# Kernel tuning notes

Hardware: AMD Instinct MI355X
Metric: run time of the kernel (lower is better)

The kernel has to match this reference:

```python
import jax, jax.numpy as jnp
import numpy as np

NUM_LAYERS = 3
CHANNELS = 8
IN_CHANNELS = 8
MASK_OUT_STRIDE = 4
WEIGHT_NUMS = [(IN_CHANNELS + 2) * CHANNELS, CHANNELS * CHANNELS, CHANNELS]
BIAS_NUMS = [CHANNELS, CHANNELS, 1]
NUM_GEN_PARAMS = sum(WEIGHT_NUMS) + sum(BIAS_NUMS)  # 169
SOI = np.array([64.0, 128.0, 256.0, 512.0, 1024.0], dtype=np.float32)


def compute_locations(h, w, stride):
    # FCOS grid point centers, (H*W, 2) in (x, y) order
    shifts_x = jnp.arange(w, dtype=jnp.float32) * stride + stride // 2
    shifts_y = jnp.arange(h, dtype=jnp.float32) * stride + stride // 2
    ys, xs = jnp.meshgrid(shifts_y, shifts_x, indexing='ij')
    return jnp.stack([xs.reshape(-1), ys.reshape(-1)], axis=1)


def parse_dynamic_params(params):
    # params: (n_inst, 169) -> per-layer weights (n, cout, cin) and biases (n, cout)
    n = params.shape[0]
    split_pts = np.cumsum(WEIGHT_NUMS + BIAS_NUMS)[:-1].tolist()
    splits = jnp.split(params, split_pts, axis=1)
    ws, bs = [], []
    for l in range(NUM_LAYERS):
        cout = CHANNELS if l < NUM_LAYERS - 1 else 1
        ws.append(splits[l].reshape(n, cout, -1))
        bs.append(splits[NUM_LAYERS + l].reshape(n, cout))
    return ws, bs


def aligned_bilinear(x, factor):
    # Faithful port of AdelaiDet aligned_bilinear (replicate pad + align_corners=True bilinear).
    if factor == 1:
        return x
    n, c, h, w = x.shape
    xp = jnp.pad(x, ((0, 0), (0, 0), (0, 1), (0, 1)), mode='edge')  # (n,c,h+1,w+1)
    oh, ow = factor * h + 1, factor * w + 1
    # align_corners=True with oh = factor*h+1 over h+1 samples -> exact coords i/factor
    ys = jnp.arange(oh, dtype=x.dtype) / factor
    xs = jnp.arange(ow, dtype=x.dtype) / factor
    y0 = jnp.floor(ys).astype(jnp.int32)
    y1 = jnp.minimum(y0 + 1, h)
    x0 = jnp.floor(xs).astype(jnp.int32)
    x1 = jnp.minimum(x0 + 1, w)
    wy = (ys - y0.astype(x.dtype))[None, None, :, None]
    wx = (xs - x0.astype(x.dtype))[None, None, None, :]
    rows = xp[:, :, y0, :] * (1 - wy) + xp[:, :, y1, :] * wy
    out = rows[:, :, :, x0] * (1 - wx) + rows[:, :, :, x1] * wx
    pad = factor // 2
    out = jnp.pad(out, ((0, 0), (0, 0), (pad, 0), (pad, 0)), mode='edge')
    return out[:, :, :oh - 1, :ow - 1]  # (n, c, factor*h, factor*w)


def dynamic_head(x, params):
    # x: (n_inst, cin, HW); per-instance 1x1 convs == batched tiny GEMMs
    ws, bs = parse_dynamic_params(params)
    h = x
    for i, (w, b) in enumerate(zip(ws, bs)):
        h = jnp.einsum('noi,nip->nop', w, h) + b[:, :, None]
        if i < NUM_LAYERS - 1:
            h = jax.nn.relu(h)
    return h  # (n_inst, 1, HW)


def setup_inputs() -> dict:
    key = jax.random.key(0)
    k = jax.random.split(key, 6)
    N, H, W, n_inst = 2, 200, 200, 128
    return {
        'mask_feats': jax.random.normal(k[0], (N, IN_CHANNELS, H, W), jnp.float32),
        'mask_head_params': jax.random.normal(k[1], (n_inst, NUM_GEN_PARAMS), jnp.float32) * 0.1,
        'boundary_head_params': jax.random.normal(k[2], (n_inst, NUM_GEN_PARAMS), jnp.float32) * 0.1,
        'instance_locations': jax.random.uniform(k[3], (n_inst, 2), jnp.float32) * 1600.0,
        'im_inds': jax.random.randint(k[4], (n_inst,), 0, N),
        'fpn_levels': jax.random.randint(k[5], (n_inst,), 0, 5),
        'mask_feat_stride': 8,
    }


def reference(mask_feats, mask_head_params, boundary_head_params, instance_locations, im_inds, fpn_levels, mask_feat_stride):
    N, C, H, W = mask_feats.shape
    n_inst = mask_head_params.shape[0]
    locs = compute_locations(H, W, mask_feat_stride)                 # (HW, 2)
    rel = instance_locations[:, None, :] - locs[None, :, :]          # (n, HW, 2)
    rel = jnp.transpose(rel, (0, 2, 1))                              # (n, 2, HW)
    soi = jnp.asarray(SOI)[fpn_levels]                               # (n,)
    rel = (rel / soi[:, None, None]).astype(mask_feats.dtype)
    feats = mask_feats[im_inds].reshape(n_inst, C, H * W)            # per-instance gather
    x = jnp.concatenate([rel, feats], axis=1)                        # (n, C+2, HW)
    factor = mask_feat_stride // MASK_OUT_STRIDE
    m = aligned_bilinear(dynamic_head(x, mask_head_params).reshape(n_inst, 1, H, W), factor)
    bd = aligned_bilinear(dynamic_head(x, boundary_head_params).reshape(n_inst, 1, H, W), factor)
    return jax.nn.sigmoid(m), jax.nn.sigmoid(bd)
```

## Files before the change

### kernel.cpp

```cpp
#include <hip/hip_runtime.h>


#define BLOCK 256
#define Hh 200
#define Ww 200
#define NP 169
#define TH 25
#define MAXR 14
#define OW 400
#define OH 400

typedef float f32x4 __attribute__((ext_vector_type(4)));
typedef float f32x2 __attribute__((ext_vector_type(2)));
typedef _Float16 f16x4 __attribute__((ext_vector_type(4)));

__device__ __forceinline__ f32x2 splat2(float v) { f32x2 r; r.x = v; r.y = v; return r; }
__device__ __forceinline__ f32x2 pkfma(f32x2 a, f32x2 b, f32x2 c) {
    return __builtin_elementwise_fma(a, b, c);
}

__global__ __launch_bounds__(BLOCK, 4) void dmh_fused(
    const float* __restrict__ mask_feats,
    const float* __restrict__ mparams,
    const float* __restrict__ bparams,
    const float* __restrict__ ilocs,
    const int*   __restrict__ im_inds,
    const int*   __restrict__ fpn_levels,
    const int*   __restrict__ stride_p,
    float* __restrict__ out,
    int n_inst)
{
    __shared__ __align__(16) float s_par[2 * 192];
    __shared__ __align__(16) _Float16 s_m[2][MAXR][Ww];

    const int tid  = threadIdx.x;
    const int tile = blockIdx.x;
    const int inst = blockIdx.y;

    for (int j = tid; j < 2 * NP; j += BLOCK) {
        const int head = (j < NP) ? 0 : 1;
        const int k = j - head * NP;
        const float v = head ? bparams[inst * NP + k] : mparams[inst * NP + k];
        int dst;
        if      (k < 80)  dst = (k / 10) * 12 + (k % 10);
        else if (k < 144) dst = 96 + (k - 80);
        else if (k < 152) dst = 160 + (k - 144);
        else if (k < 160) dst = 168 + (k - 152);
        else if (k < 168) dst = 176 + (k - 160);
        else              dst = 184;
        s_par[head * 192 + dst] = v;
    }

    const int   s    = stride_p[0];
    const int   half = s >> 1;
    const int   im   = im_inds[inst];
    const int   lvl  = fpn_levels[inst];
    const float inv_soi = 1.0f / (float)(64 << lvl);
    const float ixl = ilocs[inst * 2 + 0];
    const float iyl = ilocs[inst * 2 + 1];

    const int i0 = tile * TH;
    const int r_begin = ((i0 > 0) ? (i0 - 1) : 0) >> 1;
    int r_end = ((i0 + TH - 2) >> 1) + 1;
    if (r_end > Hh - 1) r_end = Hh - 1;
    const int nrows = r_end - r_begin + 1;

    __syncthreads();

    const int npx = nrows * Ww;
    const float* fbase = mask_feats + (size_t)im * 8 * Hh * Ww;

    for (int g = tid * 4; g < npx; g += BLOCK * 4) {
        asm volatile("" ::: "memory");

        const int lr = g / Ww;
        const int c  = g - lr * Ww;
        const int r  = r_begin + lr;

        f32x2 xa[10], xb[10];
        {
            const float ry   = (iyl - (float)(r * s + half)) * inv_soi;
            const float step = -(float)s * inv_soi;
            const float cx0  = (ixl - (float)(c * s + half)) * inv_soi;
            xa[0].x = cx0;            xa[0].y = cx0 + step;
            xb[0].x = cx0 + 2*step;   xb[0].y = cx0 + 3*step;
            xa[1] = splat2(ry);       xb[1] = xa[1];
            const float* fp = fbase + r * Ww + c;
            #pragma unroll
            for (int ch = 0; ch < 8; ch++) {
                const f32x4 f = *(const f32x4*)(fp + ch * (Hh * Ww));
                xa[2 + ch].x = f.x; xa[2 + ch].y = f.y;
                xb[2 + ch].x = f.z; xb[2 + ch].y = f.w;
            }
        }

        #pragma unroll 1
        for (int head = 0; head < 2; head++) {
            const float* P = s_par + head * 192;
            const f32x2 zero = splat2(0.0f);

            f32x2 h1a[8], h1b[8];
            #pragma unroll
            for (int o = 0; o < 8; o++) {
                const f32x4 wa = *(const f32x4*)(P + o * 12);
                const f32x4 wb = *(const f32x4*)(P + o * 12 + 4);
                const float w8 = P[o * 12 + 8];
                const float w9 = P[o * 12 + 9];
                f32x2 aa = splat2(P[168 + o]);
                f32x2 ab = aa;
                aa = pkfma(splat2(wa.x), xa[0], aa); ab = pkfma(splat2(wa.x), xb[0], ab);
                aa = pkfma(splat2(wa.y), xa[1], aa); ab = pkfma(splat2(wa.y), xb[1], ab);
                aa = pkfma(splat2(wa.z), xa[2], aa); ab = pkfma(splat2(wa.z), xb[2], ab);
                aa = pkfma(splat2(wa.w), xa[3], aa); ab = pkfma(splat2(wa.w), xb[3], ab);
                aa = pkfma(splat2(wb.x), xa[4], aa); ab = pkfma(splat2(wb.x), xb[4], ab);
                aa = pkfma(splat2(wb.y), xa[5], aa); ab = pkfma(splat2(wb.y), xb[5], ab);
                aa = pkfma(splat2(wb.z), xa[6], aa); ab = pkfma(splat2(wb.z), xb[6], ab);
                aa = pkfma(splat2(wb.w), xa[7], aa); ab = pkfma(splat2(wb.w), xb[7], ab);
                aa = pkfma(splat2(w8),   xa[8], aa); ab = pkfma(splat2(w8),   xb[8], ab);
                aa = pkfma(splat2(w9),   xa[9], aa); ab = pkfma(splat2(w9),   xb[9], ab);
                h1a[o] = __builtin_elementwise_max(aa, zero);
                h1b[o] = __builtin_elementwise_max(ab, zero);
            }

            f32x2 h2a[8], h2b[8];
            #pragma unroll
            for (int o = 0; o < 8; o++) {
                const f32x4 wa = *(const f32x4*)(P + 96 + o * 8);
                const f32x4 wb = *(const f32x4*)(P + 96 + o * 8 + 4);
                f32x2 aa = splat2(P[176 + o]);
                f32x2 ab = aa;
                aa = pkfma(splat2(wa.x), h1a[0], aa); ab = pkfma(splat2(wa.x), h1b[0], ab);
                aa = pkfma(splat2(wa.y), h1a[1], aa); ab = pkfma(splat2(wa.y), h1b[1], ab);
                aa = pkfma(splat2(wa.z), h1a[2], aa); ab = pkfma(splat2(wa.z), h1b[2], ab);
                aa = pkfma(splat2(wa.w), h1a[3], aa); ab = pkfma(splat2(wa.w), h1b[3], ab);
                aa = pkfma(splat2(wb.x), h1a[4], aa); ab = pkfma(splat2(wb.x), h1b[4], ab);
                aa = pkfma(splat2(wb.y), h1a[5], aa); ab = pkfma(splat2(wb.y), h1b[5], ab);
                aa = pkfma(splat2(wb.z), h1a[6], aa); ab = pkfma(splat2(wb.z), h1b[6], ab);
                aa = pkfma(splat2(wb.w), h1a[7], aa); ab = pkfma(splat2(wb.w), h1b[7], ab);
                h2a[o] = __builtin_elementwise_max(aa, zero);
                h2b[o] = __builtin_elementwise_max(ab, zero);
            }

            const f32x4 wa = *(const f32x4*)(P + 160);
            const f32x4 wb = *(const f32x4*)(P + 164);
            f32x2 aa = splat2(P[184]);
            f32x2 ab = aa;
            aa = pkfma(splat2(wa.x), h2a[0], aa); ab = pkfma(splat2(wa.x), h2b[0], ab);
            aa = pkfma(splat2(wa.y), h2a[1], aa); ab = pkfma(splat2(wa.y), h2b[1], ab);
            aa = pkfma(splat2(wa.z), h2a[2], aa); ab = pkfma(splat2(wa.z), h2b[2], ab);
            aa = pkfma(splat2(wa.w), h2a[3], aa); ab = pkfma(splat2(wa.w), h2b[3], ab);
            aa = pkfma(splat2(wb.x), h2a[4], aa); ab = pkfma(splat2(wb.x), h2b[4], ab);
            aa = pkfma(splat2(wb.y), h2a[5], aa); ab = pkfma(splat2(wb.y), h2b[5], ab);
            aa = pkfma(splat2(wb.z), h2a[6], aa); ab = pkfma(splat2(wb.z), h2b[6], ab);
            aa = pkfma(splat2(wb.w), h2a[7], aa); ab = pkfma(splat2(wb.w), h2b[7], ab);

            f16x4 res;
            res.x = (_Float16)aa.x; res.y = (_Float16)aa.y;
            res.z = (_Float16)ab.x; res.w = (_Float16)ab.y;
            *(f16x4*)(&s_m[head][lr][c]) = res;
        }
    }

    __syncthreads();

    float* out0 = out + (size_t)inst * (OH * OW) + (size_t)i0 * OW;
    float* out1 = out0 + (size_t)n_inst * (OH * OW);

    const float C = -1.44269504f;
    const int NU = OW / 8;
    const int ntaskb = TH * NU;
    for (int t = tid; t < ntaskb; t += BLOCK) {
        const int row = t / NU;
        const int u   = t - row * NU;
        const int i   = i0 + row;
        const int ip  = (i > 0) ? (i - 1) : 0;
        const int y0  = ip >> 1;
        const float wy = (ip & 1) ? 0.5f : 0.0f;
        const int lr0 = y0 - r_begin;
        const int r1c = (y0 + 1 <= Hh - 1) ? (y0 + 1) : (Hh - 1);
        const int lr1 = r1c - r_begin;

        #pragma unroll
        for (int head = 0; head < 2; head++) {
            const f16x4 A0h = *(const f16x4*)(&s_m[head][lr0][4 * u]);
            const f16x4 A1h = *(const f16x4*)(&s_m[head][lr1][4 * u]);
            float p0 = 0.0f, p1 = 0.0f;
            if (u > 0) {
                p0 = (float)s_m[head][lr0][4 * u - 1];
                p1 = (float)s_m[head][lr1][4 * u - 1];
            }
            float Bv[4];
            #pragma unroll
            for (int m = 0; m < 4; m++) {
                const float a0 = (float)A0h[m], a1 = (float)A1h[m];
                Bv[m] = (a0 + (a1 - a0) * wy) * C;
            }
            const float PB = (p0 + (p1 - p0) * wy) * C;

            float e[8];
            e[0] = (u > 0) ? 0.5f * (PB + Bv[0]) : Bv[0];
            e[1] = Bv[0];
            e[2] = 0.5f * (Bv[0] + Bv[1]);
            e[3] = Bv[1];
            e[4] = 0.5f * (Bv[1] + Bv[2]);
            e[5] = Bv[2];
            e[6] = 0.5f * (Bv[2] + Bv[3]);
            e[7] = Bv[3];

            f32x4 lo, hi;
            #pragma unroll
            for (int k = 0; k < 4; k++) {
                lo[k] = __builtin_amdgcn_rcpf(1.0f + __builtin_amdgcn_exp2f(e[k]));
                hi[k] = __builtin_amdgcn_rcpf(1.0f + __builtin_amdgcn_exp2f(e[4 + k]));
            }

            float* dst = (head ? out1 : out0) + row * OW + 8 * u;
            __builtin_nontemporal_store(lo, (f32x4*)dst);
            __builtin_nontemporal_store(hi, (f32x4*)(dst + 4));
        }
    }
}

extern "C" void kernel_launch(void* const* d_in, const int* in_sizes, int n_in,
                              void* d_out, int out_size, void* d_ws, size_t ws_size,
                              hipStream_t stream) {
    const float* mask_feats = (const float*)d_in[0];
    const float* mparams    = (const float*)d_in[1];
    const float* bparams    = (const float*)d_in[2];
    const float* ilocs      = (const float*)d_in[3];
    const int*   im_inds    = (const int*)d_in[4];
    const int*   fpn_levels = (const int*)d_in[5];
    const int*   stride_p   = (const int*)d_in[6];
    float* out = (float*)d_out;

    const int n_inst = in_sizes[1] / NP;
    dim3 grid(OH / TH, n_inst);
    dim3 block(BLOCK);
    hipLaunchKernelGGL(dmh_fused, grid, block, 0, stream,
                       mask_feats, mparams, bparams, ilocs,
                       im_inds, fpn_levels, stride_p, out, n_inst);
}
```

Before: 65.28 us.

## Split fused kernel into MLP pass and upsample pass via fp16 workspace

Replaces the single fused kernel, which recomputed halo rows of the low-res MLP output per tile, with two kernels. The first evaluates both dynamic-head MLPs once per low-res pixel and writes fp16 results to the workspace. The second performs the bilinear upsample and sigmoid from that buffer. This removes the redundant halo MLP work and the block-level barriers, at the cost of an extra launch and a global round-trip of the intermediate. The fused kernel remains as a fallback when the workspace is too small.

```diff
diff --git a/kernel.cpp b/kernel.cpp
--- a/kernel.cpp
+++ b/kernel.cpp
@@ -17,6 +17,202 @@
 __device__ __forceinline__ f32x2 splat2(float v) { f32x2 r; r.x = v; r.y = v; return r; }
 __device__ __forceinline__ f32x2 pkfma(f32x2 a, f32x2 b, f32x2 c) {
     return __builtin_elementwise_fma(a, b, c);
+}
+
+__device__ __forceinline__ int park_dst(int k) {
+    if (k < 80)  return (k / 10) * 12 + (k % 10);
+    if (k < 144) return 96 + (k - 80);
+    if (k < 152) return 160 + (k - 144);
+    if (k < 160) return 168 + (k - 152);
+    if (k < 168) return 176 + (k - 160);
+    return 184;
+}
+
+__device__ __forceinline__ void mlp4(const float* __restrict__ P,
+    const f32x2 (&xa)[10], const f32x2 (&xb)[10], f32x2& oa_, f32x2& ob_)
+{
+    const f32x2 zero = splat2(0.0f);
+
+    f32x2 h1a[8], h1b[8];
+    #pragma unroll
+    for (int o = 0; o < 8; o++) {
+        const f32x4 wa = *(const f32x4*)(P + o * 12);
+        const f32x4 wb = *(const f32x4*)(P + o * 12 + 4);
+        const float w8 = P[o * 12 + 8];
+        const float w9 = P[o * 12 + 9];
+        f32x2 aa = splat2(P[168 + o]);
+        f32x2 ab = aa;
+        aa = pkfma(splat2(wa.x), xa[0], aa); ab = pkfma(splat2(wa.x), xb[0], ab);
+        aa = pkfma(splat2(wa.y), xa[1], aa); ab = pkfma(splat2(wa.y), xb[1], ab);
+        aa = pkfma(splat2(wa.z), xa[2], aa); ab = pkfma(splat2(wa.z), xb[2], ab);
+        aa = pkfma(splat2(wa.w), xa[3], aa); ab = pkfma(splat2(wa.w), xb[3], ab);
+        aa = pkfma(splat2(wb.x), xa[4], aa); ab = pkfma(splat2(wb.x), xb[4], ab);
+        aa = pkfma(splat2(wb.y), xa[5], aa); ab = pkfma(splat2(wb.y), xb[5], ab);
+        aa = pkfma(splat2(wb.z), xa[6], aa); ab = pkfma(splat2(wb.z), xb[6], ab);
+        aa = pkfma(splat2(wb.w), xa[7], aa); ab = pkfma(splat2(wb.w), xb[7], ab);
+        aa = pkfma(splat2(w8),   xa[8], aa); ab = pkfma(splat2(w8),   xb[8], ab);
+        aa = pkfma(splat2(w9),   xa[9], aa); ab = pkfma(splat2(w9),   xb[9], ab);
+        h1a[o] = __builtin_elementwise_max(aa, zero);
+        h1b[o] = __builtin_elementwise_max(ab, zero);
+    }
+
+    f32x2 h2a[8], h2b[8];
+    #pragma unroll
+    for (int o = 0; o < 8; o++) {
+        const f32x4 wa = *(const f32x4*)(P + 96 + o * 8);
+        const f32x4 wb = *(const f32x4*)(P + 96 + o * 8 + 4);
+        f32x2 aa = splat2(P[176 + o]);
+        f32x2 ab = aa;
+        aa = pkfma(splat2(wa.x), h1a[0], aa); ab = pkfma(splat2(wa.x), h1b[0], ab);
+        aa = pkfma(splat2(wa.y), h1a[1], aa); ab = pkfma(splat2(wa.y), h1b[1], ab);
+        aa = pkfma(splat2(wa.z), h1a[2], aa); ab = pkfma(splat2(wa.z), h1b[2], ab);
+        aa = pkfma(splat2(wa.w), h1a[3], aa); ab = pkfma(splat2(wa.w), h1b[3], ab);
+        aa = pkfma(splat2(wb.x), h1a[4], aa); ab = pkfma(splat2(wb.x), h1b[4], ab);
+        aa = pkfma(splat2(wb.y), h1a[5], aa); ab = pkfma(splat2(wb.y), h1b[5], ab);
+        aa = pkfma(splat2(wb.z), h1a[6], aa); ab = pkfma(splat2(wb.z), h1b[6], ab);
+        aa = pkfma(splat2(wb.w), h1a[7], aa); ab = pkfma(splat2(wb.w), h1b[7], ab);
+        h2a[o] = __builtin_elementwise_max(aa, zero);
+        h2b[o] = __builtin_elementwise_max(ab, zero);
+    }
+
+    const f32x4 wa = *(const f32x4*)(P + 160);
+    const f32x4 wb = *(const f32x4*)(P + 164);
+    f32x2 aa = splat2(P[184]);
+    f32x2 ab = aa;
+    aa = pkfma(splat2(wa.x), h2a[0], aa); ab = pkfma(splat2(wa.x), h2b[0], ab);
+    aa = pkfma(splat2(wa.y), h2a[1], aa); ab = pkfma(splat2(wa.y), h2b[1], ab);
+    aa = pkfma(splat2(wa.z), h2a[2], aa); ab = pkfma(splat2(wa.z), h2b[2], ab);
+    aa = pkfma(splat2(wa.w), h2a[3], aa); ab = pkfma(splat2(wa.w), h2b[3], ab);
+    aa = pkfma(splat2(wb.x), h2a[4], aa); ab = pkfma(splat2(wb.x), h2b[4], ab);
+    aa = pkfma(splat2(wb.y), h2a[5], aa); ab = pkfma(splat2(wb.y), h2b[5], ab);
+    aa = pkfma(splat2(wb.z), h2a[6], aa); ab = pkfma(splat2(wb.z), h2b[6], ab);
+    aa = pkfma(splat2(wb.w), h2a[7], aa); ab = pkfma(splat2(wb.w), h2b[7], ab);
+    oa_ = aa; ob_ = ab;
+}
+
+__global__ __launch_bounds__(BLOCK, 4) void dmh_mlp(
+    const float* __restrict__ mask_feats,
+    const float* __restrict__ mparams,
+    const float* __restrict__ bparams,
+    const float* __restrict__ ilocs,
+    const int*   __restrict__ im_inds,
+    const int*   __restrict__ fpn_levels,
+    const int*   __restrict__ stride_p,
+    _Float16* __restrict__ mbuf)
+{
+    __shared__ __align__(16) float s_par[2 * 192];
+    const int tid   = threadIdx.x;
+    const int strip = blockIdx.x;
+    const int inst  = blockIdx.y;
+
+    for (int j = tid; j < 2 * NP; j += BLOCK) {
+        const int head = (j < NP) ? 0 : 1;
+        const int k = j - head * NP;
+        const float v = head ? bparams[inst * NP + k] : mparams[inst * NP + k];
+        s_par[head * 192 + park_dst(k)] = v;
+    }
+
+    const int   s    = stride_p[0];
+    const int   half = s >> 1;
+    const int   im   = im_inds[inst];
+    const int   lvl  = fpn_levels[inst];
+    const float inv_soi = 1.0f / (float)(64 << lvl);
+    const float ixl = ilocs[inst * 2 + 0];
+    const float iyl = ilocs[inst * 2 + 1];
+
+    __syncthreads();
+    if (tid >= 250) return;
+
+    const int px = strip * 1000 + tid * 4;
+    const int r  = px / 200;
+    const int c  = px - r * 200;
+    const float* fbase = mask_feats + (size_t)im * 8 * Hh * Ww;
+
+    f32x2 xa[10], xb[10];
+    {
+        const float ry   = (iyl - (float)(r * s + half)) * inv_soi;
+        const float step = -(float)s * inv_soi;
+        const float cx0  = (ixl - (float)(c * s + half)) * inv_soi;
+        xa[0].x = cx0;            xa[0].y = cx0 + step;
+        xb[0].x = cx0 + 2*step;   xb[0].y = cx0 + 3*step;
+        xa[1] = splat2(ry);       xb[1] = xa[1];
+        const float* fp = fbase + r * Ww + c;
+        #pragma unroll
+        for (int ch = 0; ch < 8; ch++) {
+            const f32x4 f = *(const f32x4*)(fp + ch * (Hh * Ww));
+            xa[2 + ch].x = f.x; xa[2 + ch].y = f.y;
+            xb[2 + ch].x = f.z; xb[2 + ch].y = f.w;
+        }
+    }
+
+    #pragma unroll 1
+    for (int head = 0; head < 2; head++) {
+        f32x2 oa, ob;
+        mlp4(s_par + head * 192, xa, xb, oa, ob);
+        f16x4 res;
+        res.x = (_Float16)oa.x; res.y = (_Float16)oa.y;
+        res.z = (_Float16)ob.x; res.w = (_Float16)ob.y;
+        *(f16x4*)(mbuf + ((size_t)(inst * 2 + head) * 40000 + r * 200 + c)) = res;
+    }
+}
+
+__global__ __launch_bounds__(BLOCK, 4) void dmh_upsample(
+    const _Float16* __restrict__ mbuf,
+    float* __restrict__ out, int n_inst)
+{
+    const int t = blockIdx.x * BLOCK + threadIdx.x;
+    if (t >= n_inst * 20000) return;
+    const int inst = t / 20000;
+    const int rem  = t - inst * 20000;
+    const int row  = rem / 50;
+    const int u    = rem - row * 50;
+
+    const int ip = (row > 0) ? (row - 1) : 0;
+    const int y0 = ip >> 1;
+    const int y1 = (y0 + 1 <= Hh - 1) ? (y0 + 1) : (Hh - 1);
+    const float wy = (ip & 1) ? 0.5f : 0.0f;
+    const float C = -1.44269504f;
+
+    float* out0 = out + (size_t)inst * (OH * OW) + row * OW + 8 * u;
+    float* out1 = out0 + (size_t)n_inst * (OH * OW);
+
+    #pragma unroll
+    for (int head = 0; head < 2; head++) {
+        const _Float16* m0 = mbuf + ((size_t)(inst * 2 + head) * 40000 + y0 * 200);
+        const _Float16* m1 = mbuf + ((size_t)(inst * 2 + head) * 40000 + y1 * 200);
+        const f16x4 A0 = *(const f16x4*)(m0 + 4 * u);
+        const f16x4 A1 = *(const f16x4*)(m1 + 4 * u);
+        float p0 = 0.0f, p1 = 0.0f;
+        if (u > 0) { p0 = (float)m0[4 * u - 1]; p1 = (float)m1[4 * u - 1]; }
+
+        float Bv[4];
+        #pragma unroll
+        for (int m = 0; m < 4; m++) {
+            const float a0 = (float)A0[m], a1 = (float)A1[m];
+            Bv[m] = (a0 + (a1 - a0) * wy) * C;
+        }
+        const float PB = (p0 + (p1 - p0) * wy) * C;
+
+        float e[8];
+        e[0] = (u > 0) ? 0.5f * (PB + Bv[0]) : Bv[0];
+        e[1] = Bv[0];
+        e[2] = 0.5f * (Bv[0] + Bv[1]);
+        e[3] = Bv[1];
+        e[4] = 0.5f * (Bv[1] + Bv[2]);
+        e[5] = Bv[2];
+        e[6] = 0.5f * (Bv[2] + Bv[3]);
+        e[7] = Bv[3];
+
+        f32x4 lo, hi;
+        #pragma unroll
+        for (int k = 0; k < 4; k++) {
+            lo[k] = __builtin_amdgcn_rcpf(1.0f + __builtin_amdgcn_exp2f(e[k]));
+            hi[k] = __builtin_amdgcn_rcpf(1.0f + __builtin_amdgcn_exp2f(e[4 + k]));
+        }
+        float* dst = head ? out1 : out0;
+        __builtin_nontemporal_store(lo, (f32x4*)dst);
+        __builtin_nontemporal_store(hi, (f32x4*)(dst + 4));
+    }
 }
 
 __global__ __launch_bounds__(BLOCK, 4) void dmh_fused(
@@ -41,14 +237,7 @@
         const int head = (j < NP) ? 0 : 1;
         const int k = j - head * NP;
         const float v = head ? bparams[inst * NP + k] : mparams[inst * NP + k];
-        int dst;
-        if      (k < 80)  dst = (k / 10) * 12 + (k % 10);
-        else if (k < 144) dst = 96 + (k - 80);
-        else if (k < 152) dst = 160 + (k - 144);
-        else if (k < 160) dst = 168 + (k - 152);
-        else if (k < 168) dst = 176 + (k - 160);
-        else              dst = 184;
-        s_par[head * 192 + dst] = v;
+        s_par[head * 192 + park_dst(k)] = v;
     }
 
     const int   s    = stride_p[0];
@@ -72,7 +261,6 @@
 
     for (int g = tid * 4; g < npx; g += BLOCK * 4) {
         asm volatile("" ::: "memory");
-
         const int lr = g / Ww;
         const int c  = g - lr * Ww;
         const int r  = r_begin + lr;
@@ -96,67 +284,11 @@
 
         #pragma unroll 1
         for (int head = 0; head < 2; head++) {
-            const float* P = s_par + head * 192;
-            const f32x2 zero = splat2(0.0f);
-
-            f32x2 h1a[8], h1b[8];
-            #pragma unroll
-            for (int o = 0; o < 8; o++) {
-                const f32x4 wa = *(const f32x4*)(P + o * 12);
-                const f32x4 wb = *(const f32x4*)(P + o * 12 + 4);
-                const float w8 = P[o * 12 + 8];
-                const float w9 = P[o * 12 + 9];
-                f32x2 aa = splat2(P[168 + o]);
-                f32x2 ab = aa;
-                aa = pkfma(splat2(wa.x), xa[0], aa); ab = pkfma(splat2(wa.x), xb[0], ab);
-                aa = pkfma(splat2(wa.y), xa[1], aa); ab = pkfma(splat2(wa.y), xb[1], ab);
-                aa = pkfma(splat2(wa.z), xa[2], aa); ab = pkfma(splat2(wa.z), xb[2], ab);
-                aa = pkfma(splat2(wa.w), xa[3], aa); ab = pkfma(splat2(wa.w), xb[3], ab);
-                aa = pkfma(splat2(wb.x), xa[4], aa); ab = pkfma(splat2(wb.x), xb[4], ab);
-                aa = pkfma(splat2(wb.y), xa[5], aa); ab = pkfma(splat2(wb.y), xb[5], ab);
-                aa = pkfma(splat2(wb.z), xa[6], aa); ab = pkfma(splat2(wb.z), xb[6], ab);
-                aa = pkfma(splat2(wb.w), xa[7], aa); ab = pkfma(splat2(wb.w), xb[7], ab);
-                aa = pkfma(splat2(w8),   xa[8], aa); ab = pkfma(splat2(w8),   xb[8], ab);
-                aa = pkfma(splat2(w9),   xa[9], aa); ab = pkfma(splat2(w9),   xb[9], ab);
-                h1a[o] = __builtin_elementwise_max(aa, zero);
-                h1b[o] = __builtin_elementwise_max(ab, zero);
-            }
-
-            f32x2 h2a[8], h2b[8];
-            #pragma unroll
-            for (int o = 0; o < 8; o++) {
-                const f32x4 wa = *(const f32x4*)(P + 96 + o * 8);
-                const f32x4 wb = *(const f32x4*)(P + 96 + o * 8 + 4);
-                f32x2 aa = splat2(P[176 + o]);
-                f32x2 ab = aa;
-                aa = pkfma(splat2(wa.x), h1a[0], aa); ab = pkfma(splat2(wa.x), h1b[0], ab);
-                aa = pkfma(splat2(wa.y), h1a[1], aa); ab = pkfma(splat2(wa.y), h1b[1], ab);
-                aa = pkfma(splat2(wa.z), h1a[2], aa); ab = pkfma(splat2(wa.z), h1b[2], ab);
-                aa = pkfma(splat2(wa.w), h1a[3], aa); ab = pkfma(splat2(wa.w), h1b[3], ab);
-                aa = pkfma(splat2(wb.x), h1a[4], aa); ab = pkfma(splat2(wb.x), h1b[4], ab);
-                aa = pkfma(splat2(wb.y), h1a[5], aa); ab = pkfma(splat2(wb.y), h1b[5], ab);
-                aa = pkfma(splat2(wb.z), h1a[6], aa); ab = pkfma(splat2(wb.z), h1b[6], ab);
-                aa = pkfma(splat2(wb.w), h1a[7], aa); ab = pkfma(splat2(wb.w), h1b[7], ab);
-                h2a[o] = __builtin_elementwise_max(aa, zero);
-                h2b[o] = __builtin_elementwise_max(ab, zero);
-            }
-
-            const f32x4 wa = *(const f32x4*)(P + 160);
-            const f32x4 wb = *(const f32x4*)(P + 164);
-            f32x2 aa = splat2(P[184]);
-            f32x2 ab = aa;
-            aa = pkfma(splat2(wa.x), h2a[0], aa); ab = pkfma(splat2(wa.x), h2b[0], ab);
-            aa = pkfma(splat2(wa.y), h2a[1], aa); ab = pkfma(splat2(wa.y), h2b[1], ab);
-            aa = pkfma(splat2(wa.z), h2a[2], aa); ab = pkfma(splat2(wa.z), h2b[2], ab);
-            aa = pkfma(splat2(wa.w), h2a[3], aa); ab = pkfma(splat2(wa.w), h2b[3], ab);
-            aa = pkfma(splat2(wb.x), h2a[4], aa); ab = pkfma(splat2(wb.x), h2b[4], ab);
-            aa = pkfma(splat2(wb.y), h2a[5], aa); ab = pkfma(splat2(wb.y), h2b[5], ab);
-            aa = pkfma(splat2(wb.z), h2a[6], aa); ab = pkfma(splat2(wb.z), h2b[6], ab);
-            aa = pkfma(splat2(wb.w), h2a[7], aa); ab = pkfma(splat2(wb.w), h2b[7], ab);
-
+            f32x2 oa, ob;
+            mlp4(s_par + head * 192, xa, xb, oa, ob);
             f16x4 res;
-            res.x = (_Float16)aa.x; res.y = (_Float16)aa.y;
-            res.z = (_Float16)ab.x; res.w = (_Float16)ab.y;
+            res.x = (_Float16)oa.x; res.y = (_Float16)oa.y;
+            res.z = (_Float16)ob.x; res.w = (_Float16)ob.y;
             *(f16x4*)(&s_m[head][lr][c]) = res;
         }
     }
@@ -234,9 +366,20 @@
     float* out = (float*)d_out;
 
     const int n_inst = in_sizes[1] / NP;
-    dim3 grid(OH / TH, n_inst);
-    dim3 block(BLOCK);
-    hipLaunchKernelGGL(dmh_fused, grid, block, 0, stream,
-                       mask_feats, mparams, bparams, ilocs,
-                       im_inds, fpn_levels, stride_p, out, n_inst);
-}
+    const size_t need = (size_t)n_inst * 2 * 40000 * sizeof(_Float16);
+
+    if (ws_size >= need) {
+        _Float16* mbuf = (_Float16*)d_ws;
+        hipLaunchKernelGGL(dmh_mlp, dim3(40, n_inst), dim3(BLOCK), 0, stream,
+                           mask_feats, mparams, bparams, ilocs,
+                           im_inds, fpn_levels, stride_p, mbuf);
+        const int ntask = n_inst * 20000;
+        hipLaunchKernelGGL(dmh_upsample, dim3((ntask + BLOCK - 1) / BLOCK),
+                           dim3(BLOCK), 0, stream, mbuf, out, n_inst);
+    } else {
+        dim3 grid(OH / TH, n_inst);
+        hipLaunchKernelGGL(dmh_fused, grid, dim3(BLOCK), 0, stream,
+                           mask_feats, mparams, bparams, ilocs,
+                           im_inds, fpn_levels, stride_p, out, n_inst);
+    }
+}
```

Result: slower. 104.7 us (+60.3%).
